# Kernel tuning notes

Measured on AMD Instinct MI355X. Metric: run time of the kernel, lower is better.

Reference implementation:

```python
import jax, jax.numpy as jnp
import numpy as np

B, T, D, H, L = 32, 512, 1024, 1024, 2


def setup_inputs() -> dict:
    key = jax.random.key(0)
    ks = jax.random.split(key, 8)
    s_in = 1.0 / np.sqrt(D)   # approximate orthogonal-init scale
    s_h = 1.0 / np.sqrt(H)
    return {
        "x": jax.random.normal(ks[0], (B, T, D), jnp.float32),
        "hidden": jnp.zeros((L, B, H), jnp.float32),
        "w_ih0": jax.random.normal(ks[1], (3 * H, D), jnp.float32) * s_in,
        "w_hh0": jax.random.normal(ks[2], (3 * H, H), jnp.float32) * s_h,
        "b_ih0": jnp.zeros((3 * H,), jnp.float32),
        "b_hh0": jnp.zeros((3 * H,), jnp.float32),
        "w_ih1": jax.random.normal(ks[3], (3 * H, H), jnp.float32) * s_h,
        "w_hh1": jax.random.normal(ks[4], (3 * H, H), jnp.float32) * s_h,
        "b_ih1": jnp.zeros((3 * H,), jnp.float32),
        "b_hh1": jnp.zeros((3 * H,), jnp.float32),
    }


def _gru_layer(x, h0, w_ih, w_hh, b_ih, b_hh):
    # x: [B,T,Din] -> precompute input projection once (as in source)
    xp = jnp.einsum('btd,gd->btg', x, w_ih) + b_ih        # [B,T,3H]
    xp_t = jnp.swapaxes(xp, 0, 1)                          # [T,B,3H]

    def step(h, xpt):
        hp = h @ w_hh.T + b_hh                             # [B,3H]
        r = jax.nn.sigmoid(xpt[:, :H] + hp[:, :H])
        z = jax.nn.sigmoid(xpt[:, H:2 * H] + hp[:, H:2 * H])
        n = jnp.tanh(xpt[:, 2 * H:] + r * hp[:, 2 * H:])
        h_new = (1 - z) * n + z * h
        return h_new, h_new

    h_last, ys = jax.lax.scan(step, h0, xp_t)              # ys: [T,B,H]
    return jnp.swapaxes(ys, 0, 1), h_last


def reference(x, hidden, w_ih0, w_hh0, b_ih0, b_hh0,
              w_ih1, w_hh1, b_ih1, b_hh1):
    y0, h0 = _gru_layer(x, hidden[0], w_ih0, w_hh0, b_ih0, b_hh0)
    y1, h1 = _gru_layer(y0, hidden[1], w_ih1, w_hh1, b_ih1, b_hh1)
    # dropout rates are 0.0 (eval semantics) -> identity
    return y1, jnp.stack([h0, h1], axis=0)
```

## Files before the change

kernel.cpp:

```cpp
#include <hip/hip_runtime.h>
#include <hip/hip_bf16.h>

#define NB 32
#define NT 512
#define NH 1024
#define G3 3072
#define NWG 128
#define PK_LDS 98304

typedef __attribute__((ext_vector_type(8))) short short8;
typedef __attribute__((ext_vector_type(4))) float f32x4;
typedef __attribute__((ext_vector_type(4))) unsigned short us4;
typedef unsigned long long u64;

static __device__ __forceinline__ unsigned short f2bf(float f) {
    union { float f; unsigned u; } v; v.f = f;
    if ((v.u & 0x7fffffffu) > 0x7f800000u) return (unsigned short)((v.u >> 16) | 0x0040u);
    unsigned u = v.u + 0x7fffu + ((v.u >> 16) & 1u);
    return (unsigned short)(u >> 16);
}

static __device__ __forceinline__ void coh_store8(u64* p, u64 v) {
    __hip_atomic_store(p, v, __ATOMIC_RELAXED, __HIP_MEMORY_SCOPE_AGENT);
}

static __device__ __forceinline__ void coh_issue16(const char* base, short8 o[16]) {
    asm volatile(
        "global_load_dwordx4 %0,  %16, off sc0 sc1\n\t"
        "global_load_dwordx4 %1,  %16, off offset:64 sc0 sc1\n\t"
        "global_load_dwordx4 %2,  %16, off offset:128 sc0 sc1\n\t"
        "global_load_dwordx4 %3,  %16, off offset:192 sc0 sc1\n\t"
        "global_load_dwordx4 %4,  %16, off offset:256 sc0 sc1\n\t"
        "global_load_dwordx4 %5,  %16, off offset:320 sc0 sc1\n\t"
        "global_load_dwordx4 %6,  %16, off offset:384 sc0 sc1\n\t"
        "global_load_dwordx4 %7,  %16, off offset:448 sc0 sc1\n\t"
        "global_load_dwordx4 %8,  %16, off offset:512 sc0 sc1\n\t"
        "global_load_dwordx4 %9,  %16, off offset:576 sc0 sc1\n\t"
        "global_load_dwordx4 %10, %16, off offset:640 sc0 sc1\n\t"
        "global_load_dwordx4 %11, %16, off offset:704 sc0 sc1\n\t"
        "global_load_dwordx4 %12, %16, off offset:768 sc0 sc1\n\t"
        "global_load_dwordx4 %13, %16, off offset:832 sc0 sc1\n\t"
        "global_load_dwordx4 %14, %16, off offset:896 sc0 sc1\n\t"
        "global_load_dwordx4 %15, %16, off offset:960 sc0 sc1"
        : "=&v"(o[0]), "=&v"(o[1]), "=&v"(o[2]), "=&v"(o[3]),
          "=&v"(o[4]), "=&v"(o[5]), "=&v"(o[6]), "=&v"(o[7]),
          "=&v"(o[8]), "=&v"(o[9]), "=&v"(o[10]), "=&v"(o[11]),
          "=&v"(o[12]), "=&v"(o[13]), "=&v"(o[14]), "=&v"(o[15])
        : "v"(base)
        : "memory");
}

#define VMWAIT_BIND16(NSTR, o)                                                 \
    asm volatile("s_waitcnt vmcnt(" NSTR ")"                                   \
        : "+v"(o[0]), "+v"(o[1]), "+v"(o[2]), "+v"(o[3]),                      \
          "+v"(o[4]), "+v"(o[5]), "+v"(o[6]), "+v"(o[7]),                      \
          "+v"(o[8]), "+v"(o[9]), "+v"(o[10]), "+v"(o[11]),                    \
          "+v"(o[12]), "+v"(o[13]), "+v"(o[14]), "+v"(o[15]) :: "memory");     \
    __builtin_amdgcn_sched_barrier(0)

#define MFMA_BF16 __builtin_amdgcn_mfma_f32_16x16x32_bf16

__global__ __launch_bounds__(256) void cvt_bf16_v4(const float4* __restrict__ src,
                                                   us4* __restrict__ dst, int n4) {
    for (int i = blockIdx.x * 256 + threadIdx.x; i < n4; i += gridDim.x * 256) {
        float4 v = src[i];
        us4 o;
        o.x = f2bf(v.x); o.y = f2bf(v.y); o.z = f2bf(v.z); o.w = f2bf(v.w);
        dst[i] = o;
    }
}

__global__ __launch_bounds__(256) void txp_x(const float4* __restrict__ x, us4* __restrict__ xt) {
    const int total = NT * NB * 256;
    for (int i = blockIdx.x * 256 + threadIdx.x; i < total; i += gridDim.x * 256) {
        int b = i / (NT * 256);
        int rem = i - b * (NT * 256);
        int t = rem >> 8;
        int d4 = rem & 255;
        float4 v = x[i];
        us4 o;
        o.x = f2bf(v.x); o.y = f2bf(v.y); o.z = f2bf(v.z); o.w = f2bf(v.w);
        xt[((size_t)t * NB + b) * 256 + d4] = o;
    }
}

__global__ __launch_bounds__(256) void init_h(const float* __restrict__ hid,
                                              unsigned short* __restrict__ h0b,
                                              unsigned short* __restrict__ h1b) {
    int i = blockIdx.x * 256 + threadIdx.x;
    h0b[i] = f2bf(hid[i]);
    h1b[i] = f2bf(hid[NB * NH + i]);
}

__global__ __launch_bounds__(128, 1) void gru_persistent(
    const unsigned short* __restrict__ xt,
    unsigned short* __restrict__ y0b,
    const unsigned short* __restrict__ wih0, const unsigned short* __restrict__ whh0,
    const unsigned short* __restrict__ wih1, const unsigned short* __restrict__ whh1,
    const float* __restrict__ bih0, const float* __restrict__ bhh0,
    const float* __restrict__ bih1, const float* __restrict__ bhh1,
    const float* __restrict__ hid,
    unsigned short* __restrict__ hb00, unsigned short* __restrict__ hb01,
    unsigned short* __restrict__ hb10, unsigned short* __restrict__ hb11,
    float* __restrict__ out,
    int* __restrict__ flags)
{
    extern __shared__ char lds[];
    short* blob = (short*)lds;

    const int tid  = threadIdx.x;
    const int lane = tid & 63;
    const int bh   = tid >> 6;
    const int lr   = lane & 15;
    const int lq   = lane >> 4;

    const int wg    = blockIdx.x;
    const int lay   = wg >> 6;
    const int slot  = wg & 63;
    const int j0    = slot * 16;
    const int batch = bh * 16 + lr;
    const int colg  = lq * 4;
    const int gc0   = j0 + colg;

    const int* poll_own = flags + lay * 128 + bh * 64 + lane;
    const int* poll_y0  = flags + bh * 64 + lane;
    int* pub = flags + lay * 128 + bh * 64 + slot;

    const unsigned short* wih = lay ? wih1 : wih0;
    const unsigned short* whh = lay ? whh1 : whh0;
    const float* bih = lay ? bih1 : bih0;
    const float* bhh = lay ? bhh1 : bhh0;
    unsigned short* hb[2];
    if (lay == 0) { hb[0] = hb00; hb[1] = hb01; }
    else          { hb[0] = hb10; hb[1] = hb11; }

    for (int c = tid; c < 6144; c += 128) {
        int g   = c >> 11;
        int rem = c & 2047;
        int kt  = rem >> 6;
        int q   = (rem >> 4) & 3;
        int col = rem & 15;
        *(short8*)(blob + c * 8) =
            *(const short8*)((const short*)whh + (size_t)(g * 1024 + j0 + col) * 1024 + kt * 32 + q * 8);
    }

    float br_[4], bz_[4], bxn_[4], bhn_[4];
#pragma unroll
    for (int j = 0; j < 4; ++j) {
        int gc = gc0 + j;
        br_[j]  = bih[gc] + bhh[gc];
        bz_[j]  = bih[1024 + gc] + bhh[1024 + gc];
        bxn_[j] = bih[2048 + gc];
        bhn_[j] = bhh[2048 + gc];
    }
    f32x4 hloc = *(const f32x4*)&hid[(size_t)lay * NB * NH + (size_t)batch * 1024 + gc0];

    __syncthreads();

    const short* wiA = (const short*)wih + (size_t)(j0 + lr) * 1024 + lq * 8;

    for (int t = 0; t < NT; ++t) {
        f32x4 ar  = {0.f,0.f,0.f,0.f};
        f32x4 az  = {0.f,0.f,0.f,0.f};
        f32x4 axn = {0.f,0.f,0.f,0.f};
        f32x4 ahn = {0.f,0.f,0.f,0.f};

        if (lay == 0) {
            const short* Ap = (const short*)xt + ((size_t)t * NB + batch) * 1024 + lq * 8;
#pragma unroll 8
            for (int kt = 0; kt < 32; ++kt) {
                short8 xb = *(const short8*)(Ap + kt * 32);
                short8 w0 = *(const short8*)(wiA + kt * 32);
                short8 w1 = *(const short8*)(wiA + 1048576 + kt * 32);
                short8 w2 = *(const short8*)(wiA + 2097152 + kt * 32);
                ar  = MFMA_BF16(w0, xb, ar, 0, 0, 0);
                az  = MFMA_BF16(w1, xb, az, 0, 0, 0);
                axn = MFMA_BF16(w2, xb, axn, 0, 0, 0);
            }
        } else {
            while (__hip_atomic_load(poll_y0, __ATOMIC_RELAXED, __HIP_MEMORY_SCOPE_AGENT) < t + 1)
                __builtin_amdgcn_s_sleep(2);
            asm volatile("" ::: "memory");
            short8 ya0[16], ya1[16];
            const char* yb = (const char*)y0b + (((size_t)t * NB + batch) * 1024 + lq * 8) * 2;
            coh_issue16(yb, ya0);
            coh_issue16(yb + 1024, ya1);
            VMWAIT_BIND16("16", ya0);
#pragma unroll
            for (int kt = 0; kt < 16; ++kt) {
                short8 w0 = *(const short8*)(wiA + kt * 32);
                short8 w1 = *(const short8*)(wiA + 1048576 + kt * 32);
                short8 w2 = *(const short8*)(wiA + 2097152 + kt * 32);
                ar  = MFMA_BF16(w0, ya0[kt], ar, 0, 0, 0);
                az  = MFMA_BF16(w1, ya0[kt], az, 0, 0, 0);
                axn = MFMA_BF16(w2, ya0[kt], axn, 0, 0, 0);
            }
            VMWAIT_BIND16("0", ya1);
#pragma unroll
            for (int kk = 0; kk < 16; ++kk) {
                const int kt = kk + 16;
                short8 w0 = *(const short8*)(wiA + kt * 32);
                short8 w1 = *(const short8*)(wiA + 1048576 + kt * 32);
                short8 w2 = *(const short8*)(wiA + 2097152 + kt * 32);
                ar  = MFMA_BF16(w0, ya1[kk], ar, 0, 0, 0);
                az  = MFMA_BF16(w1, ya1[kk], az, 0, 0, 0);
                axn = MFMA_BF16(w2, ya1[kk], axn, 0, 0, 0);
            }
        }

        while (__hip_atomic_load(poll_own, __ATOMIC_RELAXED, __HIP_MEMORY_SCOPE_AGENT) < t)
            __builtin_amdgcn_s_sleep(2);
        asm volatile("" ::: "memory");
        {
            short8 ha0[16], ha1[16];
            const char* hbase = (const char*)hb[t & 1] + ((size_t)batch * 1024 + lq * 8) * 2;
            coh_issue16(hbase, ha0);
            coh_issue16(hbase + 1024, ha1);
            VMWAIT_BIND16("16", ha0);
#pragma unroll
            for (int kt = 0; kt < 16; ++kt) {
                short8 b0 = *(const short8*)(blob + kt * 512 + lane * 8);
                short8 b1 = *(const short8*)(blob + (32 + kt) * 512 + lane * 8);
                short8 b2 = *(const short8*)(blob + (64 + kt) * 512 + lane * 8);
                ar  = MFMA_BF16(b0, ha0[kt], ar, 0, 0, 0);
                az  = MFMA_BF16(b1, ha0[kt], az, 0, 0, 0);
                ahn = MFMA_BF16(b2, ha0[kt], ahn, 0, 0, 0);
            }
            VMWAIT_BIND16("0", ha1);
#pragma unroll
            for (int kk = 0; kk < 16; ++kk) {
                const int kt = kk + 16;
                short8 b0 = *(const short8*)(blob + kt * 512 + lane * 8);
                short8 b1 = *(const short8*)(blob + (32 + kt) * 512 + lane * 8);
                short8 b2 = *(const short8*)(blob + (64 + kt) * 512 + lane * 8);
                ar  = MFMA_BF16(b0, ha1[kk], ar, 0, 0, 0);
                az  = MFMA_BF16(b1, ha1[kk], az, 0, 0, 0);
                ahn = MFMA_BF16(b2, ha1[kk], ahn, 0, 0, 0);
            }
        }

        u64 hpack = 0;
        float hv[4];
#pragma unroll
        for (int j = 0; j < 4; ++j) {
            float r  = 1.f / (1.f + __expf(-(ar[j] + br_[j])));
            float z  = 1.f / (1.f + __expf(-(az[j] + bz_[j])));
            float na = axn[j] + bxn_[j] + r * (ahn[j] + bhn_[j]);
            float e2 = __expf(-2.f * na);
            float n  = (1.f - e2) / (1.f + e2);
            float h  = (1.f - z) * n + z * hloc[j];
            hloc[j] = h;
            hv[j] = h;
            hpack |= (u64)f2bf(h) << (16 * j);
        }
        coh_store8((u64*)((unsigned short*)hb[(t + 1) & 1] + (size_t)batch * 1024 + gc0), hpack);
        if (lay == 0)
            coh_store8((u64*)(y0b + ((size_t)t * NB + batch) * 1024 + gc0), hpack);

        asm volatile("s_waitcnt vmcnt(0)" ::: "memory");
        if (lane == 0)
            __hip_atomic_store(pub, t + 1, __ATOMIC_RELAXED, __HIP_MEMORY_SCOPE_AGENT);

        if (lay == 1) {
            float4 o4; o4.x = hv[0]; o4.y = hv[1]; o4.z = hv[2]; o4.w = hv[3];
            *(float4*)&out[((size_t)batch * NT + t) * 1024 + gc0] = o4;
        }
        if (t == NT - 1) {
            float4 o4; o4.x = hv[0]; o4.y = hv[1]; o4.z = hv[2]; o4.w = hv[3];
            *(float4*)&out[(size_t)NB * NT * 1024 + (size_t)lay * NB * NH + (size_t)batch * 1024 + gc0] = o4;
        }
    }
}

extern "C" void kernel_launch(void* const* d_in, const int* in_sizes, int n_in,
                              void* d_out, int out_size, void* d_ws, size_t ws_size,
                              hipStream_t stream) {
    (void)in_sizes; (void)n_in; (void)out_size; (void)ws_size;

    const float* x     = (const float*)d_in[0];
    const float* hid   = (const float*)d_in[1];
    const float* w_ih0 = (const float*)d_in[2];
    const float* w_hh0 = (const float*)d_in[3];
    const float* b_ih0 = (const float*)d_in[4];
    const float* b_hh0 = (const float*)d_in[5];
    const float* w_ih1 = (const float*)d_in[6];
    const float* w_hh1 = (const float*)d_in[7];
    const float* b_ih1 = (const float*)d_in[8];
    const float* b_hh1 = (const float*)d_in[9];
    float* out = (float*)d_out;

    char* ws = (char*)d_ws;
    size_t off = 0;
    auto alloc = [&](size_t bytes) -> void* {
        void* p = ws + off;
        off += (bytes + 255) & ~(size_t)255;
        return p;
    };

    unsigned short* xtb   = (unsigned short*)alloc((size_t)NT * NB * 1024 * 2);
    unsigned short* y0b   = (unsigned short*)alloc((size_t)NT * NB * 1024 * 2);
    unsigned short* wih0b = (unsigned short*)alloc((size_t)G3 * 1024 * 2);
    unsigned short* whh0b = (unsigned short*)alloc((size_t)G3 * 1024 * 2);
    unsigned short* wih1b = (unsigned short*)alloc((size_t)G3 * 1024 * 2);
    unsigned short* whh1b = (unsigned short*)alloc((size_t)G3 * 1024 * 2);
    unsigned short* hb0[2]; unsigned short* hb1[2];
    for (int i = 0; i < 2; i++) hb0[i] = (unsigned short*)alloc(NB * NH * 2);
    for (int i = 0; i < 2; i++) hb1[i] = (unsigned short*)alloc(NB * NH * 2);
    int* flags = (int*)alloc(2 * 2 * 64 * sizeof(int));

    txp_x<<<2048, 256, 0, stream>>>((const float4*)x, (us4*)xtb);
    cvt_bf16_v4<<<512, 256, 0, stream>>>((const float4*)w_ih0, (us4*)wih0b, G3 * 1024 / 4);
    cvt_bf16_v4<<<512, 256, 0, stream>>>((const float4*)w_hh0, (us4*)whh0b, G3 * 1024 / 4);
    cvt_bf16_v4<<<512, 256, 0, stream>>>((const float4*)w_ih1, (us4*)wih1b, G3 * 1024 / 4);
    cvt_bf16_v4<<<512, 256, 0, stream>>>((const float4*)w_hh1, (us4*)whh1b, G3 * 1024 / 4);
    init_h<<<NB * NH / 256, 256, 0, stream>>>(hid, hb0[0], hb1[0]);
    hipMemsetAsync(flags, 0, 2 * 2 * 64 * sizeof(int), stream);

    (void)hipFuncSetAttribute((const void*)gru_persistent,
                              hipFuncAttributeMaxDynamicSharedMemorySize, PK_LDS);
    gru_persistent<<<NWG, 128, PK_LDS, stream>>>(
        xtb, y0b, wih0b, whh0b, wih1b, whh1b,
        b_ih0, b_hh0, b_ih1, b_hh1, hid,
        hb0[0], hb0[1], hb1[0], hb1[1],
        out, flags);
}
```

Baseline: 8.001 ms.

## Replace flag-based sync with sentinel-filled per-timestep hidden-state slots

Drops the per-step flag publish and poll protocol. Each timestep's hidden state now goes to its own slot in a full history buffer that is pre-filled with 0xFF, and readers poll the data itself, reloading any chunk that still holds the all-ones sentinel. The history is stored in an MFMA-fragment layout so each lane reads contiguous 16-byte chunks. Layer 0 now converts x from fp32 inline instead of using a separate transpose and convert pre-pass. The cost is large memsets over the history buffers and a correctness reliance on no real bf16 data forming the 0xFFFFFFFF pattern. Ordering between the four dwords of one chunk is also not guaranteed.

```diff
diff --git a/kernel.cpp b/kernel.cpp
--- a/kernel.cpp
+++ b/kernel.cpp
@@ -5,58 +5,61 @@
 #define NT 512
 #define NH 1024
 #define G3 3072
-#define NWG 128
 #define PK_LDS 98304
+#define TSLOT 65536
 
 typedef __attribute__((ext_vector_type(8))) short short8;
 typedef __attribute__((ext_vector_type(4))) float f32x4;
 typedef __attribute__((ext_vector_type(4))) unsigned short us4;
 typedef unsigned long long u64;
 
-static __device__ __forceinline__ unsigned short f2bf(float f) {
+static __device__ __forceinline__ unsigned short f2bf_r(float f) {
     union { float f; unsigned u; } v; v.f = f;
-    if ((v.u & 0x7fffffffu) > 0x7f800000u) return (unsigned short)((v.u >> 16) | 0x0040u);
-    unsigned u = v.u + 0x7fffu + ((v.u >> 16) & 1u);
-    return (unsigned short)(u >> 16);
-}
-
-static __device__ __forceinline__ void coh_store8(u64* p, u64 v) {
-    __hip_atomic_store(p, v, __ATOMIC_RELAXED, __HIP_MEMORY_SCOPE_AGENT);
-}
-
-static __device__ __forceinline__ void coh_issue16(const char* base, short8 o[16]) {
-    asm volatile(
-        "global_load_dwordx4 %0,  %16, off sc0 sc1\n\t"
-        "global_load_dwordx4 %1,  %16, off offset:64 sc0 sc1\n\t"
-        "global_load_dwordx4 %2,  %16, off offset:128 sc0 sc1\n\t"
-        "global_load_dwordx4 %3,  %16, off offset:192 sc0 sc1\n\t"
-        "global_load_dwordx4 %4,  %16, off offset:256 sc0 sc1\n\t"
-        "global_load_dwordx4 %5,  %16, off offset:320 sc0 sc1\n\t"
-        "global_load_dwordx4 %6,  %16, off offset:384 sc0 sc1\n\t"
-        "global_load_dwordx4 %7,  %16, off offset:448 sc0 sc1\n\t"
-        "global_load_dwordx4 %8,  %16, off offset:512 sc0 sc1\n\t"
-        "global_load_dwordx4 %9,  %16, off offset:576 sc0 sc1\n\t"
-        "global_load_dwordx4 %10, %16, off offset:640 sc0 sc1\n\t"
-        "global_load_dwordx4 %11, %16, off offset:704 sc0 sc1\n\t"
-        "global_load_dwordx4 %12, %16, off offset:768 sc0 sc1\n\t"
-        "global_load_dwordx4 %13, %16, off offset:832 sc0 sc1\n\t"
-        "global_load_dwordx4 %14, %16, off offset:896 sc0 sc1\n\t"
-        "global_load_dwordx4 %15, %16, off offset:960 sc0 sc1"
-        : "=&v"(o[0]), "=&v"(o[1]), "=&v"(o[2]), "=&v"(o[3]),
-          "=&v"(o[4]), "=&v"(o[5]), "=&v"(o[6]), "=&v"(o[7]),
-          "=&v"(o[8]), "=&v"(o[9]), "=&v"(o[10]), "=&v"(o[11]),
-          "=&v"(o[12]), "=&v"(o[13]), "=&v"(o[14]), "=&v"(o[15])
-        : "v"(base)
-        : "memory");
-}
+    return (unsigned short)((v.u + 0x7fffu + ((v.u >> 16) & 1u)) >> 16);
+}
+
+static __device__ __forceinline__ void st8_llc(u64* p, u64 v) {
+    asm volatile("global_store_dwordx2 %0, %1, off sc0 sc1" :: "v"(p), "v"(v) : "memory");
+}
+
+static __device__ __forceinline__ bool chunk_bad(short8 s) {
+    union { short8 s; uint4 u; } c; c.s = s;
+    return (c.u.x == ~0u) || (c.u.y == ~0u) || (c.u.z == ~0u) || (c.u.w == ~0u);
+}
+
+#define LOAD4(arr, i0, bp)                                                     \
+    asm volatile(                                                              \
+        "global_load_dwordx4 %0, %4, off sc0 sc1\n\t"                          \
+        "global_load_dwordx4 %1, %4, off offset:1024 sc0 sc1\n\t"              \
+        "global_load_dwordx4 %2, %4, off offset:2048 sc0 sc1\n\t"              \
+        "global_load_dwordx4 %3, %4, off offset:3072 sc0 sc1"                  \
+        : "=&v"(arr[i0]), "=&v"(arr[i0+1]), "=&v"(arr[i0+2]), "=&v"(arr[i0+3]) \
+        : "v"(bp) : "memory")
 
 #define VMWAIT_BIND16(NSTR, o)                                                 \
     asm volatile("s_waitcnt vmcnt(" NSTR ")"                                   \
-        : "+v"(o[0]), "+v"(o[1]), "+v"(o[2]), "+v"(o[3]),                      \
-          "+v"(o[4]), "+v"(o[5]), "+v"(o[6]), "+v"(o[7]),                      \
-          "+v"(o[8]), "+v"(o[9]), "+v"(o[10]), "+v"(o[11]),                    \
-          "+v"(o[12]), "+v"(o[13]), "+v"(o[14]), "+v"(o[15]) :: "memory");     \
+        : "+v"((o)[0]), "+v"((o)[1]), "+v"((o)[2]), "+v"((o)[3]),              \
+          "+v"((o)[4]), "+v"((o)[5]), "+v"((o)[6]), "+v"((o)[7]),              \
+          "+v"((o)[8]), "+v"((o)[9]), "+v"((o)[10]), "+v"((o)[11]),            \
+          "+v"((o)[12]), "+v"((o)[13]), "+v"((o)[14]), "+v"((o)[15]) :: "memory"); \
     __builtin_amdgcn_sched_barrier(0)
+
+#define RELOAD1(dst, bp)                                                       \
+    asm volatile("global_load_dwordx4 %0, %1, off sc0 sc1\n\ts_waitcnt vmcnt(0)" \
+        : "=&v"(dst) : "v"(bp) : "memory");                                    \
+    __builtin_amdgcn_sched_barrier(0)
+
+#define SEQ_READ32(arr, basep)                                                 \
+    do {                                                                       \
+        _Pragma("unroll")                                                      \
+        for (int g_ = 0; g_ < 8; ++g_) { const char* bp_ = (basep) + g_ * 4096; LOAD4(arr, g_ * 4, bp_); } \
+        VMWAIT_BIND16("0", arr);                                               \
+        VMWAIT_BIND16("0", (arr) + 16);                                        \
+        _Pragma("unroll")                                                      \
+        for (int i_ = 0; i_ < 32; ++i_) {                                      \
+            while (__any(chunk_bad(arr[i_]))) { RELOAD1(arr[i_], (basep) + i_ * 1024); } \
+        }                                                                      \
+    } while (0)
 
 #define MFMA_BF16 __builtin_amdgcn_mfma_f32_16x16x32_bf16
 
@@ -65,45 +68,36 @@
     for (int i = blockIdx.x * 256 + threadIdx.x; i < n4; i += gridDim.x * 256) {
         float4 v = src[i];
         us4 o;
-        o.x = f2bf(v.x); o.y = f2bf(v.y); o.z = f2bf(v.z); o.w = f2bf(v.w);
+        o.x = f2bf_r(v.x); o.y = f2bf_r(v.y); o.z = f2bf_r(v.z); o.w = f2bf_r(v.w);
         dst[i] = o;
     }
 }
 
-__global__ __launch_bounds__(256) void txp_x(const float4* __restrict__ x, us4* __restrict__ xt) {
-    const int total = NT * NB * 256;
-    for (int i = blockIdx.x * 256 + threadIdx.x; i < total; i += gridDim.x * 256) {
-        int b = i / (NT * 256);
-        int rem = i - b * (NT * 256);
-        int t = rem >> 8;
-        int d4 = rem & 255;
-        float4 v = x[i];
-        us4 o;
-        o.x = f2bf(v.x); o.y = f2bf(v.y); o.z = f2bf(v.z); o.w = f2bf(v.w);
-        xt[((size_t)t * NB + b) * 256 + d4] = o;
-    }
-}
-
-__global__ __launch_bounds__(256) void init_h(const float* __restrict__ hid,
-                                              unsigned short* __restrict__ h0b,
-                                              unsigned short* __restrict__ h1b) {
+__global__ __launch_bounds__(256) void init_h_blob(const float* __restrict__ hid,
+                                                   unsigned short* __restrict__ hseq0,
+                                                   unsigned short* __restrict__ hseq1) {
     int i = blockIdx.x * 256 + threadIdx.x;
-    h0b[i] = f2bf(hid[i]);
-    h1b[i] = f2bf(hid[NB * NH + i]);
-}
-
-__global__ __launch_bounds__(128, 1) void gru_persistent(
-    const unsigned short* __restrict__ xt,
-    unsigned short* __restrict__ y0b,
+    int lay = i >> 12, rem = i & 4095;
+    int b = rem >> 7, co = rem & 127;
+    const float* src = hid + (size_t)lay * NB * NH + (size_t)b * 1024 + co * 8;
+    unsigned short* base = lay ? hseq1 : hseq0;
+    int kt = co >> 2, o = co & 3, bh = b >> 4, lr = b & 15;
+    unsigned short* dst = base + bh * 16384 + kt * 512 + (o * 16 + lr) * 8;
+    us4 v0, v1;
+    v0.x = f2bf_r(src[0]); v0.y = f2bf_r(src[1]); v0.z = f2bf_r(src[2]); v0.w = f2bf_r(src[3]);
+    v1.x = f2bf_r(src[4]); v1.y = f2bf_r(src[5]); v1.z = f2bf_r(src[6]); v1.w = f2bf_r(src[7]);
+    ((us4*)dst)[0] = v0; ((us4*)dst)[1] = v1;
+}
+
+__global__ __launch_bounds__(128, 1) void gru_seq(
+    const float* __restrict__ x,
     const unsigned short* __restrict__ wih0, const unsigned short* __restrict__ whh0,
     const unsigned short* __restrict__ wih1, const unsigned short* __restrict__ whh1,
     const float* __restrict__ bih0, const float* __restrict__ bhh0,
     const float* __restrict__ bih1, const float* __restrict__ bhh1,
     const float* __restrict__ hid,
-    unsigned short* __restrict__ hb00, unsigned short* __restrict__ hb01,
-    unsigned short* __restrict__ hb10, unsigned short* __restrict__ hb11,
-    float* __restrict__ out,
-    int* __restrict__ flags)
+    char* __restrict__ hseq0, char* __restrict__ hseq1,
+    float* __restrict__ out)
 {
     extern __shared__ char lds[];
     short* blob = (short*)lds;
@@ -119,27 +113,17 @@
     const int slot  = wg & 63;
     const int j0    = slot * 16;
     const int batch = bh * 16 + lr;
-    const int colg  = lq * 4;
-    const int gc0   = j0 + colg;
-
-    const int* poll_own = flags + lay * 128 + bh * 64 + lane;
-    const int* poll_y0  = flags + bh * 64 + lane;
-    int* pub = flags + lay * 128 + bh * 64 + slot;
+    const int gc0   = j0 + lq * 4;
 
     const unsigned short* wih = lay ? wih1 : wih0;
     const unsigned short* whh = lay ? whh1 : whh0;
     const float* bih = lay ? bih1 : bih0;
     const float* bhh = lay ? bhh1 : bhh0;
-    unsigned short* hb[2];
-    if (lay == 0) { hb[0] = hb00; hb[1] = hb01; }
-    else          { hb[0] = hb10; hb[1] = hb11; }
+    char* hseq = lay ? hseq1 : hseq0;
 
     for (int c = tid; c < 6144; c += 128) {
-        int g   = c >> 11;
-        int rem = c & 2047;
-        int kt  = rem >> 6;
-        int q   = (rem >> 4) & 3;
-        int col = rem & 15;
+        int g = c >> 11, rem = c & 2047;
+        int kt = rem >> 6, q = (rem >> 4) & 3, col = rem & 15;
         *(short8*)(blob + c * 8) =
             *(const short8*)((const short*)whh + (size_t)(g * 1024 + j0 + col) * 1024 + kt * 32 + q * 8);
     }
@@ -158,6 +142,10 @@
     __syncthreads();
 
     const short* wiA = (const short*)wih + (size_t)(j0 + lr) * 1024 + lq * 8;
+    const char* rd_base_off = (const char*)0 + (size_t)bh * 32768 + (size_t)lane * 16;
+    const int kt_w = slot >> 1;
+    const int o_w  = (slot & 1) * 2 + (lq >> 1);
+    const size_t wr_off = (size_t)bh * 32768 + (size_t)kt_w * 1024 + (size_t)(o_w * 16 + lr) * 16 + (size_t)(lq & 1) * 8;
 
     for (int t = 0; t < NT; ++t) {
         f32x4 ar  = {0.f,0.f,0.f,0.f};
@@ -166,76 +154,50 @@
         f32x4 ahn = {0.f,0.f,0.f,0.f};
 
         if (lay == 0) {
-            const short* Ap = (const short*)xt + ((size_t)t * NB + batch) * 1024 + lq * 8;
+            const float* xb = x + ((size_t)batch * NT + t) * 1024 + lq * 8;
 #pragma unroll 8
             for (int kt = 0; kt < 32; ++kt) {
-                short8 xb = *(const short8*)(Ap + kt * 32);
+                float4 a0 = *(const float4*)(xb + kt * 32);
+                float4 a1 = *(const float4*)(xb + kt * 32 + 4);
+                short8 xf;
+                xf[0] = (short)f2bf_r(a0.x); xf[1] = (short)f2bf_r(a0.y);
+                xf[2] = (short)f2bf_r(a0.z); xf[3] = (short)f2bf_r(a0.w);
+                xf[4] = (short)f2bf_r(a1.x); xf[5] = (short)f2bf_r(a1.y);
+                xf[6] = (short)f2bf_r(a1.z); xf[7] = (short)f2bf_r(a1.w);
                 short8 w0 = *(const short8*)(wiA + kt * 32);
                 short8 w1 = *(const short8*)(wiA + 1048576 + kt * 32);
                 short8 w2 = *(const short8*)(wiA + 2097152 + kt * 32);
-                ar  = MFMA_BF16(w0, xb, ar, 0, 0, 0);
-                az  = MFMA_BF16(w1, xb, az, 0, 0, 0);
-                axn = MFMA_BF16(w2, xb, axn, 0, 0, 0);
+                ar  = MFMA_BF16(w0, xf, ar, 0, 0, 0);
+                az  = MFMA_BF16(w1, xf, az, 0, 0, 0);
+                axn = MFMA_BF16(w2, xf, axn, 0, 0, 0);
             }
         } else {
-            while (__hip_atomic_load(poll_y0, __ATOMIC_RELAXED, __HIP_MEMORY_SCOPE_AGENT) < t + 1)
-                __builtin_amdgcn_s_sleep(2);
-            asm volatile("" ::: "memory");
-            short8 ya0[16], ya1[16];
-            const char* yb = (const char*)y0b + (((size_t)t * NB + batch) * 1024 + lq * 8) * 2;
-            coh_issue16(yb, ya0);
-            coh_issue16(yb + 1024, ya1);
-            VMWAIT_BIND16("16", ya0);
-#pragma unroll
-            for (int kt = 0; kt < 16; ++kt) {
+            short8 pf[32];
+            const char* pb = hseq0 + (size_t)(t + 1) * TSLOT + (size_t)(rd_base_off - (const char*)0);
+            SEQ_READ32(pf, pb);
+#pragma unroll 8
+            for (int kt = 0; kt < 32; ++kt) {
                 short8 w0 = *(const short8*)(wiA + kt * 32);
                 short8 w1 = *(const short8*)(wiA + 1048576 + kt * 32);
                 short8 w2 = *(const short8*)(wiA + 2097152 + kt * 32);
-                ar  = MFMA_BF16(w0, ya0[kt], ar, 0, 0, 0);
-                az  = MFMA_BF16(w1, ya0[kt], az, 0, 0, 0);
-                axn = MFMA_BF16(w2, ya0[kt], axn, 0, 0, 0);
+                ar  = MFMA_BF16(w0, pf[kt], ar, 0, 0, 0);
+                az  = MFMA_BF16(w1, pf[kt], az, 0, 0, 0);
+                axn = MFMA_BF16(w2, pf[kt], axn, 0, 0, 0);
             }
-            VMWAIT_BIND16("0", ya1);
-#pragma unroll
-            for (int kk = 0; kk < 16; ++kk) {
-                const int kt = kk + 16;
-                short8 w0 = *(const short8*)(wiA + kt * 32);
-                short8 w1 = *(const short8*)(wiA + 1048576 + kt * 32);
-                short8 w2 = *(const short8*)(wiA + 2097152 + kt * 32);
-                ar  = MFMA_BF16(w0, ya1[kk], ar, 0, 0, 0);
-                az  = MFMA_BF16(w1, ya1[kk], az, 0, 0, 0);
-                axn = MFMA_BF16(w2, ya1[kk], axn, 0, 0, 0);
-            }
-        }
-
-        while (__hip_atomic_load(poll_own, __ATOMIC_RELAXED, __HIP_MEMORY_SCOPE_AGENT) < t)
-            __builtin_amdgcn_s_sleep(2);
-        asm volatile("" ::: "memory");
+        }
+
         {
-            short8 ha0[16], ha1[16];
-            const char* hbase = (const char*)hb[t & 1] + ((size_t)batch * 1024 + lq * 8) * 2;
-            coh_issue16(hbase, ha0);
-            coh_issue16(hbase + 1024, ha1);
-            VMWAIT_BIND16("16", ha0);
-#pragma unroll
-            for (int kt = 0; kt < 16; ++kt) {
-                short8 b0 = *(const short8*)(blob + kt * 512 + lane * 8);
-                short8 b1 = *(const short8*)(blob + (32 + kt) * 512 + lane * 8);
-                short8 b2 = *(const short8*)(blob + (64 + kt) * 512 + lane * 8);
-                ar  = MFMA_BF16(b0, ha0[kt], ar, 0, 0, 0);
-                az  = MFMA_BF16(b1, ha0[kt], az, 0, 0, 0);
-                ahn = MFMA_BF16(b2, ha0[kt], ahn, 0, 0, 0);
-            }
-            VMWAIT_BIND16("0", ha1);
-#pragma unroll
-            for (int kk = 0; kk < 16; ++kk) {
-                const int kt = kk + 16;
-                short8 b0 = *(const short8*)(blob + kt * 512 + lane * 8);
-                short8 b1 = *(const short8*)(blob + (32 + kt) * 512 + lane * 8);
-                short8 b2 = *(const short8*)(blob + (64 + kt) * 512 + lane * 8);
-                ar  = MFMA_BF16(b0, ha1[kk], ar, 0, 0, 0);
-                az  = MFMA_BF16(b1, ha1[kk], az, 0, 0, 0);
-                ahn = MFMA_BF16(b2, ha1[kk], ahn, 0, 0, 0);
+            short8 hf[32];
+            const char* hb = hseq + (size_t)t * TSLOT + (size_t)(rd_base_off - (const char*)0);
+            SEQ_READ32(hf, hb);
+#pragma unroll 8
+            for (int kt = 0; kt < 32; ++kt) {
+                short8 c0 = *(const short8*)(blob + kt * 512 + lane * 8);
+                short8 c1 = *(const short8*)(blob + (32 + kt) * 512 + lane * 8);
+                short8 c2 = *(const short8*)(blob + (64 + kt) * 512 + lane * 8);
+                ar  = MFMA_BF16(c0, hf[kt], ar, 0, 0, 0);
+                az  = MFMA_BF16(c1, hf[kt], az, 0, 0, 0);
+                ahn = MFMA_BF16(c2, hf[kt], ahn, 0, 0, 0);
             }
         }
 
@@ -249,17 +211,10 @@
             float e2 = __expf(-2.f * na);
             float n  = (1.f - e2) / (1.f + e2);
             float h  = (1.f - z) * n + z * hloc[j];
-            hloc[j] = h;
-            hv[j] = h;
-            hpack |= (u64)f2bf(h) << (16 * j);
-        }
-        coh_store8((u64*)((unsigned short*)hb[(t + 1) & 1] + (size_t)batch * 1024 + gc0), hpack);
-        if (lay == 0)
-            coh_store8((u64*)(y0b + ((size_t)t * NB + batch) * 1024 + gc0), hpack);
-
-        asm volatile("s_waitcnt vmcnt(0)" ::: "memory");
-        if (lane == 0)
-            __hip_atomic_store(pub, t + 1, __ATOMIC_RELAXED, __HIP_MEMORY_SCOPE_AGENT);
+            hloc[j] = h; hv[j] = h;
+            hpack |= (u64)f2bf_r(h) << (16 * j);
+        }
+        st8_llc((u64*)(hseq + (size_t)(t + 1) * TSLOT + wr_off), hpack);
 
         if (lay == 1) {
             float4 o4; o4.x = hv[0]; o4.y = hv[1]; o4.z = hv[2]; o4.w = hv[3];
@@ -297,30 +252,26 @@
         return p;
     };
 
-    unsigned short* xtb   = (unsigned short*)alloc((size_t)NT * NB * 1024 * 2);
-    unsigned short* y0b   = (unsigned short*)alloc((size_t)NT * NB * 1024 * 2);
     unsigned short* wih0b = (unsigned short*)alloc((size_t)G3 * 1024 * 2);
     unsigned short* whh0b = (unsigned short*)alloc((size_t)G3 * 1024 * 2);
     unsigned short* wih1b = (unsigned short*)alloc((size_t)G3 * 1024 * 2);
     unsigned short* whh1b = (unsigned short*)alloc((size_t)G3 * 1024 * 2);
-    unsigned short* hb0[2]; unsigned short* hb1[2];
-    for (int i = 0; i < 2; i++) hb0[i] = (unsigned short*)alloc(NB * NH * 2);
-    for (int i = 0; i < 2; i++) hb1[i] = (unsigned short*)alloc(NB * NH * 2);
-    int* flags = (int*)alloc(2 * 2 * 64 * sizeof(int));
-
-    txp_x<<<2048, 256, 0, stream>>>((const float4*)x, (us4*)xtb);
+    char* hseq0 = (char*)alloc((size_t)(NT + 1) * TSLOT);
+    char* hseq1 = (char*)alloc((size_t)(NT + 1) * TSLOT);
+
+    hipMemsetAsync(hseq0 + TSLOT, 0xFF, (size_t)NT * TSLOT, stream);
+    hipMemsetAsync(hseq1 + TSLOT, 0xFF, (size_t)NT * TSLOT, stream);
+
     cvt_bf16_v4<<<512, 256, 0, stream>>>((const float4*)w_ih0, (us4*)wih0b, G3 * 1024 / 4);
     cvt_bf16_v4<<<512, 256, 0, stream>>>((const float4*)w_hh0, (us4*)whh0b, G3 * 1024 / 4);
     cvt_bf16_v4<<<512, 256, 0, stream>>>((const float4*)w_ih1, (us4*)wih1b, G3 * 1024 / 4);
     cvt_bf16_v4<<<512, 256, 0, stream>>>((const float4*)w_hh1, (us4*)whh1b, G3 * 1024 / 4);
-    init_h<<<NB * NH / 256, 256, 0, stream>>>(hid, hb0[0], hb1[0]);
-    hipMemsetAsync(flags, 0, 2 * 2 * 64 * sizeof(int), stream);
-
-    (void)hipFuncSetAttribute((const void*)gru_persistent,
+    init_h_blob<<<32, 256, 0, stream>>>(hid, (unsigned short*)hseq0, (unsigned short*)hseq1);
+
+    (void)hipFuncSetAttribute((const void*)gru_seq,
                               hipFuncAttributeMaxDynamicSharedMemorySize, PK_LDS);
-    gru_persistent<<<NWG, 128, PK_LDS, stream>>>(
-        xtb, y0b, wih0b, whh0b, wih1b, whh1b,
+    gru_seq<<<128, 128, PK_LDS, stream>>>(
+        x, wih0b, whh0b, wih1b, whh1b,
         b_ih0, b_hh0, b_ih1, b_hh1, hid,
-        hb0[0], hb0[1], hb1[0], hb1[1],
-        out, flags);
-}
+        hseq0, hseq1, out);
+}
```

After: 9.916 ms. 23.9% more time.

## Precompute layer-0 input projection with a batched GEMM outside the recurrent loop

Applied to the files above, without the earlier changes.

Layer-0's input projection no longer runs as per-timestep MFMA work inside the persistent kernel. A separate tiled bf16 MFMA GEMM computes x·W_ih0ᵀ+b for all timesteps up front and stores it in bf16, and each step of the recurrent kernel just loads its slice. Weight conversion for w_hh is folded into the persistent kernel's LDS load, which removes several conversion launches. Spin-waits also drop s_sleep, trading more polling traffic for lower wake-up latency. The precomputed projection now holds bf16 rounding of the pre-activation, and the GEMM adds a large extra write and read of intermediate data.

```diff
diff --git a/kernel.cpp b/kernel.cpp
--- a/kernel.cpp
+++ b/kernel.cpp
@@ -13,11 +13,21 @@
 typedef __attribute__((ext_vector_type(4))) unsigned short us4;
 typedef unsigned long long u64;
 
-static __device__ __forceinline__ unsigned short f2bf(float f) {
+static __device__ __forceinline__ unsigned short f2bf_r(float f) {
     union { float f; unsigned u; } v; v.f = f;
-    if ((v.u & 0x7fffffffu) > 0x7f800000u) return (unsigned short)((v.u >> 16) | 0x0040u);
-    unsigned u = v.u + 0x7fffu + ((v.u >> 16) & 1u);
-    return (unsigned short)(u >> 16);
+    return (unsigned short)((v.u + 0x7fffu + ((v.u >> 16) & 1u)) >> 16);
+}
+static __device__ __forceinline__ float bf2f(unsigned short s) {
+    union { unsigned u; float f; } v; v.u = ((unsigned)s) << 16; return v.f;
+}
+static __device__ __forceinline__ short8 cvt8(const float* p) {
+    float4 a0 = *(const float4*)p, a1 = *(const float4*)(p + 4);
+    short8 v;
+    v[0] = (short)f2bf_r(a0.x); v[1] = (short)f2bf_r(a0.y);
+    v[2] = (short)f2bf_r(a0.z); v[3] = (short)f2bf_r(a0.w);
+    v[4] = (short)f2bf_r(a1.x); v[5] = (short)f2bf_r(a1.y);
+    v[6] = (short)f2bf_r(a1.z); v[7] = (short)f2bf_r(a1.w);
+    return v;
 }
 
 static __device__ __forceinline__ void coh_store8(u64* p, u64 v) {
@@ -65,22 +75,8 @@
     for (int i = blockIdx.x * 256 + threadIdx.x; i < n4; i += gridDim.x * 256) {
         float4 v = src[i];
         us4 o;
-        o.x = f2bf(v.x); o.y = f2bf(v.y); o.z = f2bf(v.z); o.w = f2bf(v.w);
+        o.x = f2bf_r(v.x); o.y = f2bf_r(v.y); o.z = f2bf_r(v.z); o.w = f2bf_r(v.w);
         dst[i] = o;
-    }
-}
-
-__global__ __launch_bounds__(256) void txp_x(const float4* __restrict__ x, us4* __restrict__ xt) {
-    const int total = NT * NB * 256;
-    for (int i = blockIdx.x * 256 + threadIdx.x; i < total; i += gridDim.x * 256) {
-        int b = i / (NT * 256);
-        int rem = i - b * (NT * 256);
-        int t = rem >> 8;
-        int d4 = rem & 255;
-        float4 v = x[i];
-        us4 o;
-        o.x = f2bf(v.x); o.y = f2bf(v.y); o.z = f2bf(v.z); o.w = f2bf(v.w);
-        xt[((size_t)t * NB + b) * 256 + d4] = o;
     }
 }
 
@@ -88,16 +84,67 @@
                                               unsigned short* __restrict__ h0b,
                                               unsigned short* __restrict__ h1b) {
     int i = blockIdx.x * 256 + threadIdx.x;
-    h0b[i] = f2bf(hid[i]);
-    h1b[i] = f2bf(hid[NB * NH + i]);
+    h0b[i] = f2bf_r(hid[i]);
+    h1b[i] = f2bf_r(hid[NB * NH + i]);
+}
+
+__global__ __launch_bounds__(256) void gemm_nt_f32(const float* __restrict__ A,
+                                                   const float* __restrict__ W,
+                                                   const float* __restrict__ bias,
+                                                   unsigned short* __restrict__ C, int M, int N) {
+    __shared__ short As[128][40];
+    __shared__ short Bs[128][40];
+    int tid = threadIdx.x;
+    int nblk = N >> 7;
+    int bn = blockIdx.x % nblk, bm = blockIdx.x / nblk;
+    int lane = tid & 63, w = tid >> 6;
+    int wm = w >> 1, wn = w & 1;
+    int lr = lane & 15, lk = lane >> 4;
+    f32x4 acc[4][4];
+#pragma unroll
+    for (int i = 0; i < 4; i++)
+#pragma unroll
+        for (int j = 0; j < 4; j++) acc[i][j] = (f32x4){0.f,0.f,0.f,0.f};
+    int r0 = tid >> 2, kc = (tid & 3) * 8;
+    for (int k0 = 0; k0 < 1024; k0 += 32) {
+        __syncthreads();
+#pragma unroll
+        for (int jj = 0; jj < 2; jj++) {
+            int row = r0 + jj * 64;
+            *(short8*)&As[row][kc] = cvt8(&A[(size_t)(bm * 128 + row) * 1024 + k0 + kc]);
+            *(short8*)&Bs[row][kc] = cvt8(&W[(size_t)(bn * 128 + row) * 1024 + k0 + kc]);
+        }
+        __syncthreads();
+        short8 af[4], bf[4];
+#pragma unroll
+        for (int mi = 0; mi < 4; mi++) af[mi] = *(const short8*)&As[wm * 64 + mi * 16 + lr][lk * 8];
+#pragma unroll
+        for (int ni = 0; ni < 4; ni++) bf[ni] = *(const short8*)&Bs[wn * 64 + ni * 16 + lr][lk * 8];
+#pragma unroll
+        for (int mi = 0; mi < 4; mi++)
+#pragma unroll
+            for (int ni = 0; ni < 4; ni++)
+                acc[mi][ni] = MFMA_BF16(af[mi], bf[ni], acc[mi][ni], 0, 0, 0);
+    }
+#pragma unroll
+    for (int mi = 0; mi < 4; mi++)
+#pragma unroll
+        for (int ni = 0; ni < 4; ni++) {
+            int gr = bm * 128 + wm * 64 + mi * 16 + lk * 4;
+            int gc = bn * 128 + wn * 64 + ni * 16 + lr;
+            float bv = bias[gc];
+#pragma unroll
+            for (int r = 0; r < 4; r++)
+                C[(size_t)(gr + r) * N + gc] = f2bf_r(acc[mi][ni][r] + bv);
+        }
 }
 
 __global__ __launch_bounds__(128, 1) void gru_persistent(
-    const unsigned short* __restrict__ xt,
+    const unsigned short* __restrict__ xp0,
     unsigned short* __restrict__ y0b,
-    const unsigned short* __restrict__ wih0, const unsigned short* __restrict__ whh0,
-    const unsigned short* __restrict__ wih1, const unsigned short* __restrict__ whh1,
-    const float* __restrict__ bih0, const float* __restrict__ bhh0,
+    const unsigned short* __restrict__ wih1b,
+    const float* __restrict__ whh0, const float* __restrict__ whh1,
+    const float* __restrict__ bhh0,
     const float* __restrict__ bih1, const float* __restrict__ bhh1,
     const float* __restrict__ hid,
     unsigned short* __restrict__ hb00, unsigned short* __restrict__ hb01,
@@ -119,70 +166,64 @@
     const int slot  = wg & 63;
     const int j0    = slot * 16;
     const int batch = bh * 16 + lr;
-    const int colg  = lq * 4;
-    const int gc0   = j0 + colg;
+    const int gc0   = j0 + lq * 4;
 
     const int* poll_own = flags + lay * 128 + bh * 64 + lane;
     const int* poll_y0  = flags + bh * 64 + lane;
     int* pub = flags + lay * 128 + bh * 64 + slot;
 
-    const unsigned short* wih = lay ? wih1 : wih0;
-    const unsigned short* whh = lay ? whh1 : whh0;
-    const float* bih = lay ? bih1 : bih0;
-    const float* bhh = lay ? bhh1 : bhh0;
+    const float* whh = lay ? whh1 : whh0;
     unsigned short* hb[2];
     if (lay == 0) { hb[0] = hb00; hb[1] = hb01; }
     else          { hb[0] = hb10; hb[1] = hb11; }
 
     for (int c = tid; c < 6144; c += 128) {
-        int g   = c >> 11;
-        int rem = c & 2047;
-        int kt  = rem >> 6;
-        int q   = (rem >> 4) & 3;
-        int col = rem & 15;
+        int g = c >> 11, rem = c & 2047;
+        int kt = rem >> 6, q = (rem >> 4) & 3, col = rem & 15;
         *(short8*)(blob + c * 8) =
-            *(const short8*)((const short*)whh + (size_t)(g * 1024 + j0 + col) * 1024 + kt * 32 + q * 8);
+            cvt8(whh + (size_t)(g * 1024 + j0 + col) * 1024 + kt * 32 + q * 8);
     }
 
     float br_[4], bz_[4], bxn_[4], bhn_[4];
 #pragma unroll
     for (int j = 0; j < 4; ++j) {
         int gc = gc0 + j;
-        br_[j]  = bih[gc] + bhh[gc];
-        bz_[j]  = bih[1024 + gc] + bhh[1024 + gc];
-        bxn_[j] = bih[2048 + gc];
-        bhn_[j] = bhh[2048 + gc];
+        if (lay == 0) {
+            br_[j]  = bhh0[gc];
+            bz_[j]  = bhh0[1024 + gc];
+            bxn_[j] = 0.f;
+            bhn_[j] = bhh0[2048 + gc];
+        } else {
+            br_[j]  = bih1[gc] + bhh1[gc];
+            bz_[j]  = bih1[1024 + gc] + bhh1[1024 + gc];
+            bxn_[j] = bih1[2048 + gc];
+            bhn_[j] = bhh1[2048 + gc];
+        }
     }
     f32x4 hloc = *(const f32x4*)&hid[(size_t)lay * NB * NH + (size_t)batch * 1024 + gc0];
 
     __syncthreads();
 
-    const short* wiA = (const short*)wih + (size_t)(j0 + lr) * 1024 + lq * 8;
+    const short* wiA = (const short*)wih1b + (size_t)(j0 + lr) * 1024 + lq * 8;
+    const size_t aoff_b = (((size_t)(bh * 16 + lr)) * 1024 + lq * 8) * 2;
 
     for (int t = 0; t < NT; ++t) {
         f32x4 ar  = {0.f,0.f,0.f,0.f};
         f32x4 az  = {0.f,0.f,0.f,0.f};
         f32x4 axn = {0.f,0.f,0.f,0.f};
         f32x4 ahn = {0.f,0.f,0.f,0.f};
+        u64 xpr = 0, xpz = 0, xpn = 0;
 
         if (lay == 0) {
-            const short* Ap = (const short*)xt + ((size_t)t * NB + batch) * 1024 + lq * 8;
-#pragma unroll 8
-            for (int kt = 0; kt < 32; ++kt) {
-                short8 xb = *(const short8*)(Ap + kt * 32);
-                short8 w0 = *(const short8*)(wiA + kt * 32);
-                short8 w1 = *(const short8*)(wiA + 1048576 + kt * 32);
-                short8 w2 = *(const short8*)(wiA + 2097152 + kt * 32);
-                ar  = MFMA_BF16(w0, xb, ar, 0, 0, 0);
-                az  = MFMA_BF16(w1, xb, az, 0, 0, 0);
-                axn = MFMA_BF16(w2, xb, axn, 0, 0, 0);
-            }
+            const unsigned short* xpp = xp0 + ((size_t)batch * NT + t) * G3 + gc0;
+            xpr = *(const u64*)xpp;
+            xpz = *(const u64*)(xpp + 1024);
+            xpn = *(const u64*)(xpp + 2048);
         } else {
-            while (__hip_atomic_load(poll_y0, __ATOMIC_RELAXED, __HIP_MEMORY_SCOPE_AGENT) < t + 1)
-                __builtin_amdgcn_s_sleep(2);
+            while (__hip_atomic_load(poll_y0, __ATOMIC_RELAXED, __HIP_MEMORY_SCOPE_AGENT) < t + 1) { }
             asm volatile("" ::: "memory");
             short8 ya0[16], ya1[16];
-            const char* yb = (const char*)y0b + (((size_t)t * NB + batch) * 1024 + lq * 8) * 2;
+            const char* yb = (const char*)y0b + ((size_t)t * NB) * 2048 + aoff_b;
             coh_issue16(yb, ya0);
             coh_issue16(yb + 1024, ya1);
             VMWAIT_BIND16("16", ya0);
@@ -208,12 +249,11 @@
             }
         }
 
-        while (__hip_atomic_load(poll_own, __ATOMIC_RELAXED, __HIP_MEMORY_SCOPE_AGENT) < t)
-            __builtin_amdgcn_s_sleep(2);
+        while (__hip_atomic_load(poll_own, __ATOMIC_RELAXED, __HIP_MEMORY_SCOPE_AGENT) < t) { }
         asm volatile("" ::: "memory");
         {
             short8 ha0[16], ha1[16];
-            const char* hbase = (const char*)hb[t & 1] + ((size_t)batch * 1024 + lq * 8) * 2;
+            const char* hbase = (const char*)hb[t & 1] + aoff_b;
             coh_issue16(hbase, ha0);
             coh_issue16(hbase + 1024, ha1);
             VMWAIT_BIND16("16", ha0);
@@ -243,15 +283,20 @@
         float hv[4];
 #pragma unroll
         for (int j = 0; j < 4; ++j) {
-            float r  = 1.f / (1.f + __expf(-(ar[j] + br_[j])));
-            float z  = 1.f / (1.f + __expf(-(az[j] + bz_[j])));
-            float na = axn[j] + bxn_[j] + r * (ahn[j] + bhn_[j]);
+            float xr, xz, xn;
+            if (lay == 0) {
+                xr = bf2f((unsigned short)(xpr >> (16 * j)));
+                xz = bf2f((unsigned short)(xpz >> (16 * j)));
+                xn = bf2f((unsigned short)(xpn >> (16 * j)));
+            } else { xr = 0.f; xz = 0.f; xn = axn[j]; }
+            float r  = 1.f / (1.f + __expf(-(xr + ar[j] + br_[j])));
+            float z  = 1.f / (1.f + __expf(-(xz + az[j] + bz_[j])));
+            float na = xn + bxn_[j] + r * (ahn[j] + bhn_[j]);
             float e2 = __expf(-2.f * na);
             float n  = (1.f - e2) / (1.f + e2);
             float h  = (1.f - z) * n + z * hloc[j];
-            hloc[j] = h;
-            hv[j] = h;
-            hpack |= (u64)f2bf(h) << (16 * j);
+            hloc[j] = h; hv[j] = h;
+            hpack |= (u64)f2bf_r(h) << (16 * j);
         }
         coh_store8((u64*)((unsigned short*)hb[(t + 1) & 1] + (size_t)batch * 1024 + gc0), hpack);
         if (lay == 0)
@@ -297,30 +342,25 @@
         return p;
     };
 
-    unsigned short* xtb   = (unsigned short*)alloc((size_t)NT * NB * 1024 * 2);
+    const size_t M = (size_t)NB * NT;
+    unsigned short* xp0   = (unsigned short*)alloc(M * G3 * 2);
     unsigned short* y0b   = (unsigned short*)alloc((size_t)NT * NB * 1024 * 2);
-    unsigned short* wih0b = (unsigned short*)alloc((size_t)G3 * 1024 * 2);
-    unsigned short* whh0b = (unsigned short*)alloc((size_t)G3 * 1024 * 2);
     unsigned short* wih1b = (unsigned short*)alloc((size_t)G3 * 1024 * 2);
-    unsigned short* whh1b = (unsigned short*)alloc((size_t)G3 * 1024 * 2);
     unsigned short* hb0[2]; unsigned short* hb1[2];
     for (int i = 0; i < 2; i++) hb0[i] = (unsigned short*)alloc(NB * NH * 2);
     for (int i = 0; i < 2; i++) hb1[i] = (unsigned short*)alloc(NB * NH * 2);
-    int* flags = (int*)alloc(2 * 2 * 64 * sizeof(int));
-
-    txp_x<<<2048, 256, 0, stream>>>((const float4*)x, (us4*)xtb);
-    cvt_bf16_v4<<<512, 256, 0, stream>>>((const float4*)w_ih0, (us4*)wih0b, G3 * 1024 / 4);
-    cvt_bf16_v4<<<512, 256, 0, stream>>>((const float4*)w_hh0, (us4*)whh0b, G3 * 1024 / 4);
+    int* flags = (int*)alloc(2048);
+
+    gemm_nt_f32<<<(int)(M / 128) * (G3 / 128), 256, 0, stream>>>(x, w_ih0, b_ih0, xp0, (int)M, G3);
     cvt_bf16_v4<<<512, 256, 0, stream>>>((const float4*)w_ih1, (us4*)wih1b, G3 * 1024 / 4);
-    cvt_bf16_v4<<<512, 256, 0, stream>>>((const float4*)w_hh1, (us4*)whh1b, G3 * 1024 / 4);
     init_h<<<NB * NH / 256, 256, 0, stream>>>(hid, hb0[0], hb1[0]);
-    hipMemsetAsync(flags, 0, 2 * 2 * 64 * sizeof(int), stream);
+    hipMemsetAsync(flags, 0, 2048, stream);
 
     (void)hipFuncSetAttribute((const void*)gru_persistent,
                               hipFuncAttributeMaxDynamicSharedMemorySize, PK_LDS);
     gru_persistent<<<NWG, 128, PK_LDS, stream>>>(
-        xtb, y0b, wih0b, whh0b, wih1b, whh1b,
-        b_ih0, b_hh0, b_ih1, b_hh1, hid,
+        xp0, y0b, wih1b, w_hh0, w_hh1,
+        b_hh0, b_ih1, b_hh1, hid,
         hb0[0], hb0[1], hb1[0], hb1[1],
         out, flags);
 }
```

Result: slower. 9.579 ms (+19.7%).
